# Kernel tuning notes

Measured on AMD Instinct MI355X. Metric: run time of the kernel, lower is better.

Reference implementation:

```python
import jax, jax.numpy as jnp
import numpy as np

B, D, T, G = 8, 40, 192, 256
UNITS, DEMO, OUT = 256, 16, 1


def setup_inputs() -> dict:
    key = jax.random.key(0)
    ks = jax.random.split(key, 10)
    # observation timestamps, sorted, shared across channels (per preprocessing tile)
    t1 = jnp.sort(jax.random.uniform(ks[0], (B, T)) * 48.0, axis=-1)
    times = jnp.broadcast_to(t1[:, None, :], (B, D, T))
    values = jax.random.normal(ks[1], (B, D, T))
    meas = (jax.random.uniform(ks[2], (B, D, T)) < 0.5).astype(jnp.float32)
    meas = meas.at[:, :, 0].set(1.0)  # guarantee >=1 observation per channel
    grid = jnp.broadcast_to(jnp.linspace(0.0, 48.0, G)[None, :], (B, G))
    grid_lengths = jnp.concatenate([
        jax.random.randint(ks[3], (B - 1,), G // 2, G + 1, dtype=jnp.int32),
        jnp.array([G], dtype=jnp.int32)])
    demo = jax.random.normal(ks[4], (B, DEMO))
    # learned parameters
    kernel_sic = jnp.zeros((D,))                       # softplus-param RBF widths
    cross_W = jnp.eye(D)                               # identity init
    demo_W1 = jax.random.normal(ks[5], (DEMO, UNITS)) * 0.1
    demo_b1 = jnp.zeros((UNITS,))
    demo_W2 = jax.random.normal(ks[6], (UNITS, UNITS)) * 0.05
    demo_b2 = jnp.zeros((UNITS,))
    gru_Wx = jax.random.normal(ks[7], (3 * D, 3 * UNITS)) * 0.05
    gru_Wh = jax.random.normal(ks[8], (UNITS, 3 * UNITS)) * 0.05
    gru_b = jnp.zeros((2, 3 * UNITS))                  # keras reset_after=True: [input_bias, recurrent_bias]
    out_W = jax.random.normal(ks[9], (UNITS, OUT)) * 0.1
    out_b = jnp.zeros((OUT,))
    return dict(demo=demo, times=times, values=values, measurements=meas,
                grid=grid, kernel_sic=kernel_sic, cross_W=cross_W,
                demo_W1=demo_W1, demo_b1=demo_b1, demo_W2=demo_W2, demo_b2=demo_b2,
                gru_Wx=gru_Wx, gru_Wh=gru_Wh, gru_b=gru_b,
                out_W=out_W, out_b=out_b, grid_lengths=grid_lengths)


def _forward(demo, times, values, meas, grid, kernel_sic, cross_W,
             demo_W1, demo_b1, demo_W2, demo_b2,
             gru_Wx, gru_Wh, gru_b, out_W, out_b, grid_lengths):
    # ---- single_channel_interp (reconstruction=False) ----
    logmask = jnp.where(meas > 0, 0.0, -jnp.inf)[:, :, :, None]   # [B,D,T,1]
    norm = (times[:, :, :, None] - grid[:, None, None, :]) ** 2   # [B,D,T,G]
    alpha = jax.nn.softplus(kernel_sic)[None, :, None, None]      # [1,D,1,1]

    def interp(scale):
        logits = -scale * alpha * norm + logmask                  # [B,D,T,G]
        w = jax.nn.logsumexp(logits, axis=2)                      # [B,D,G]
        p = jnp.exp(logits - w[:, :, None, :])                    # softmax over T
        y = jnp.sum(p * values[:, :, :, None], axis=2)            # [B,D,G]
        return y, w

    y, w = interp(1.0)            # smooth interpolant + log-intensity
    y_trans, _ = interp(10.0)     # sharper (transient) interpolant

    # ---- cross_channel_interp (reconstruction=False) ----
    yT = jnp.swapaxes(y, 1, 2)                                    # [B,G,D]
    wT = jnp.swapaxes(w, 1, 2)
    sw = jax.nn.softmax(wT, axis=2)                               # softmax over channels
    mean = jnp.mean(yT, axis=1, keepdims=True)                    # [B,1,D]
    rep = jnp.einsum('bgd,de->bge', sw * (yT - mean), cross_W) + mean
    rep1 = jnp.swapaxes(rep, 1, 2)                                # [B,D,G]
    intensity = jnp.exp(w)
    feats = jnp.concatenate([rep1, intensity, y_trans - rep1], axis=1)  # [B,3D,G]
    rnn_in = jnp.swapaxes(feats, 1, 2)                            # [B,G,3D]

    # ---- demo encoder -> GRU initial state ----
    h0 = jax.nn.relu(demo @ demo_W1 + demo_b1) @ demo_W2 + demo_b2

    # ---- masked GRU (keras v2, reset_after=True), return last state ----
    bi, br = gru_b[0], gru_b[1]
    Gn = rnn_in.shape[1]
    seq_mask = jnp.arange(Gn)[None, :] < grid_lengths[:, None]    # [B,G]
    x_proj = rnn_in @ gru_Wx + bi                                 # [B,G,3U]

    def step(h, inp):
        xp, m = inp                                               # [B,3U], [B]
        hp = h @ gru_Wh + br
        xz, xr, xh = jnp.split(xp, 3, axis=-1)
        hz, hr, hh = jnp.split(hp, 3, axis=-1)
        z = jax.nn.sigmoid(xz + hz)
        r = jax.nn.sigmoid(xr + hr)
        cand = jnp.tanh(xh + r * hh)
        h_new = z * h + (1.0 - z) * cand
        return jnp.where(m[:, None], h_new, h), None

    h_final, _ = jax.lax.scan(step, h0,
                              (jnp.swapaxes(x_proj, 0, 1), seq_mask.T))
    return jax.nn.sigmoid(h_final @ out_W + out_b)                # [B,OUT]


def reference(demo, times, values, measurements, grid, kernel_sic, cross_W,
              demo_W1, demo_b1, demo_W2, demo_b2,
              gru_Wx, gru_Wh, gru_b, out_W, out_b, grid_lengths):
    return _forward(demo, times, values, measurements, grid, kernel_sic, cross_W,
                    demo_W1, demo_b1, demo_W2, demo_b2,
                    gru_Wx, gru_Wh, gru_b, out_W, out_b, grid_lengths)
```

## Files before the change

### kernel.cpp

```cpp
#include <hip/hip_runtime.h>
#include <hip/hip_bf16.h>

#define B_ 8
#define D_ 40
#define T_ 192
#define G_ 256
#define U_ 768
#define H_ 256

#define PINV(x) asm volatile("" : "+v"(x))

__device__ inline float sigmoidf_(float x){
  return 1.0f/(1.0f+__expf(-x));
}
__device__ inline float tanhf_(float x){
  float ax = fabsf(x);
  float e = __expf(-2.0f*ax);
  float t = (1.0f-e)/(1.0f+e);
  return copysignf(t, x);
}
__device__ inline int sdot4(int a, int b, int c){
#if __has_builtin(__builtin_amdgcn_sdot4)
  return __builtin_amdgcn_sdot4(a, b, c, false);
#else
  int r = c;
  #pragma unroll
  for (int i=0;i<4;i++){
    int ai = (a << (24-8*i)) >> 24;
    int bi = (b << (24-8*i)) >> 24;
    r += ai*bi;
  }
  return r;
#endif
}
__device__ inline int pack4(int q0,int q1,int q2,int q3){
  return (q0&255) | ((q1&255)<<8) | ((q2&255)<<16) | ((q3&255)<<24);
}

__global__ __launch_bounds__(256) void k_interp(
    const float* __restrict__ times, const float* __restrict__ values,
    const float* __restrict__ meas, const float* __restrict__ grid,
    const float* __restrict__ ksic,
    float* __restrict__ y, float* __restrict__ w, float* __restrict__ ytr,
    float* __restrict__ mean){
  int bd = blockIdx.x;
  int b = bd / D_, d = bd % D_;
  int g = threadIdx.x;
  __shared__ float tt[T_], vv[T_], mm[T_];
  __shared__ float red[256];
  if (g < T_){
    tt[g] = times[bd*T_+g];
    vv[g] = values[bd*T_+g];
    mm[g] = meas[bd*T_+g];
  }
  __syncthreads();
  float alpha = log1pf(__expf(ksic[d]));
  float tg = grid[b*G_+g];
  float nmin = 3.4e38f;
  for (int t=0;t<T_;t++){
    if (mm[t] > 0.0f){
      float dd = tt[t]-tg;
      nmin = fminf(nmin, dd*dd);
    }
  }
  float s1=0.f, sv1=0.f, s10=0.f, sv10=0.f;
  for (int t=0;t<T_;t++){
    if (mm[t] > 0.0f){
      float dd = tt[t]-tg;
      float n = dd*dd - nmin;
      float e1  = __expf(-alpha*n);
      float e10 = __expf(-10.0f*alpha*n);
      s1 += e1;  sv1 += e1*vv[t];
      s10 += e10; sv10 += e10*vv[t];
    }
  }
  float yv = sv1/s1;
  float wv = -alpha*nmin + __logf(s1);
  y[bd*G_+g]   = yv;
  w[bd*G_+g]   = wv;
  ytr[bd*G_+g] = sv10/s10;
  red[g] = yv;
  __syncthreads();
  for (int s=128;s>0;s>>=1){
    if (g<s) red[g]+=red[g+s];
    __syncthreads();
  }
  if (g==0) mean[bd] = red[0]*(1.0f/(float)G_);
}

__global__ __launch_bounds__(256) void k_cross(
    const float* __restrict__ y, const float* __restrict__ w,
    const float* __restrict__ ytr, const float* __restrict__ mean,
    const float* __restrict__ crossW, const float* __restrict__ Wx,
    const float* __restrict__ gru_b, const int* __restrict__ lens,
    float* __restrict__ xproj){
  int blk = blockIdx.x;
  int b = blk >> 6, gq = blk & 63;
  int g0 = gq*4;
  if (g0 >= lens[b]) return;
  __shared__ float wd[4][D_], yd[4][D_], ytrd[4][D_], md[D_];
  __shared__ float cc4[4][D_], feats[4][3*D_];
  __shared__ float wstat[4][2];
  int tid = threadIdx.x;
  int gg = tid / D_;
  int d  = tid % D_;
  if (tid < 4*D_){
    int idx = (b*D_+d)*G_ + g0 + gg;
    wd[gg][d]=w[idx]; yd[gg][d]=y[idx]; ytrd[gg][d]=ytr[idx];
  }
  if (tid < D_) md[tid] = mean[b*D_+tid];
  __syncthreads();
  if (tid < 4){
    float mx=-3.4e38f;
    for (int d2=0;d2<D_;d2++) mx = fmaxf(mx, wd[tid][d2]);
    float s=0.f;
    for (int d2=0;d2<D_;d2++) s += __expf(wd[tid][d2]-mx);
    wstat[tid][0]=mx; wstat[tid][1]=1.0f/s;
  }
  __syncthreads();
  if (tid < 4*D_){
    float sw = __expf(wd[gg][d]-wstat[gg][0])*wstat[gg][1];
    cc4[gg][d] = sw*(yd[gg][d]-md[d]);
  }
  __syncthreads();
  if (tid < 4*D_){
    float acc=0.f;
    for (int d2=0;d2<D_;d2++) acc += cc4[gg][d2]*crossW[d2*D_+d];
    float rep = acc + md[d];
    feats[gg][d]       = rep;
    feats[gg][D_+d]    = __expf(wd[gg][d]);
    feats[gg][2*D_+d]  = ytrd[gg][d]-rep;
  }
  __syncthreads();
  for (int jj=0;jj<3;jj++){
    int j = tid + jj*256;
    float bi = gru_b[j];
    float a0=bi, a1=bi, a2=bi, a3=bi;
    #pragma unroll 4
    for (int i=0;i<3*D_;i++){
      float wv = Wx[i*U_+j];
      a0 += feats[0][i]*wv;
      a1 += feats[1][i]*wv;
      a2 += feats[2][i]*wv;
      a3 += feats[3][i]*wv;
    }
    size_t base = ((size_t)(b*G_+g0))*U_ + j;
    xproj[base]       = a0;
    xproj[base+U_]    = a1;
    xproj[base+2*U_]  = a2;
    xproj[base+3*U_]  = a3;
  }
}

__global__ __launch_bounds__(256) void k_demo(
    const float* __restrict__ demo, const float* __restrict__ W1,
    const float* __restrict__ b1, const float* __restrict__ W2,
    const float* __restrict__ b2, float* __restrict__ h0){
  __shared__ float dl[B_*16];
  __shared__ float hid[B_*H_];
  int u = threadIdx.x;
  if (u < B_*16) dl[u] = demo[u];
  __syncthreads();
  float acc[B_];
  #pragma unroll
  for (int b=0;b<B_;b++) acc[b]=b1[u];
  for (int i=0;i<16;i++){
    float w1 = W1[i*H_+u];
    #pragma unroll
    for (int b=0;b<B_;b++) acc[b] += dl[b*16+i]*w1;
  }
  #pragma unroll
  for (int b=0;b<B_;b++) hid[b*H_+u] = fmaxf(acc[b],0.f);
  __syncthreads();
  #pragma unroll
  for (int b=0;b<B_;b++) acc[b]=b2[u];
  for (int k=0;k<H_;k++){
    float w2 = W2[k*H_+u];
    #pragma unroll
    for (int b=0;b<B_;b++) acc[b] += hid[b*H_+k]*w2;
  }
  #pragma unroll
  for (int b=0;b<B_;b++) h0[b*H_+u]=acc[b];
}

__global__ __launch_bounds__(256) void k_quant(
    const float* __restrict__ Wh, int* __restrict__ wsq,
    float* __restrict__ wmaxs){
  int c0 = blockIdx.x*64;
  int rg = threadIdx.x >> 6;
  int cc = threadIdx.x & 63;
  int col = c0 + cc;
  float v[64];
  float mx = 0.f;
  #pragma unroll
  for (int r=0;r<64;r++){
    v[r] = Wh[(size_t)(rg*64+r)*U_ + col];
    mx = fmaxf(mx, fabsf(v[r]));
  }
  __shared__ float cm[4][64];
  cm[rg][cc] = mx;
  __syncthreads();
  float m = fmaxf(fmaxf(cm[0][cc],cm[1][cc]), fmaxf(cm[2][cc],cm[3][cc]));
  float iw = (m>0.f)? 127.0f/m : 0.f;
  if (rg==0) wmaxs[col] = m;
  #pragma unroll
  for (int k=0;k<16;k++){
    int q0=(int)rintf(v[4*k+0]*iw), q1=(int)rintf(v[4*k+1]*iw),
        q2=(int)rintf(v[4*k+2]*iw), q3=(int)rintf(v[4*k+3]*iw);
    wsq[(size_t)(rg*16+k)*U_ + col] = pack4(q0,q1,q2,q3);
  }
}

__global__ __attribute__((amdgpu_flat_work_group_size(256,256), amdgpu_waves_per_eu(1,1)))
void k_gru(
    const int* __restrict__ wsq, const float* __restrict__ wmaxs,
    const float* __restrict__ gru_b,
    const float* __restrict__ xproj, const float* __restrict__ h0,
    const int* __restrict__ lens, const float* __restrict__ outW,
    const float* __restrict__ outb, float* __restrict__ out){
  int b = blockIdx.x;
  int j = threadIdx.x;

  __shared__ __align__(16) int hq[2][64];
  __shared__ float red[H_];
  __shared__ float shs[2];

  float hj = h0[b*H_+j];
  red[j] = fabsf(hj);
  __syncthreads();
  for (int st=128; st>0; st>>=1){
    if (j < st) red[j] = fmaxf(red[j], red[j+st]);
    __syncthreads();
  }
  if (j==0){
    float bound = fmaxf(red[0], 1.0f);
    shs[0] = 127.0f/bound;
    shs[1] = bound/127.0f;
  }
  __syncthreads();
  float inv_sh = shs[0];
  float s_h    = shs[1];

  float cm0 = wmaxs[j], cm1 = wmaxs[H_+j], cm2 = wmaxs[2*H_+j];
  float fz = (cm0*(1.0f/127.0f))*s_h;
  float fr = (cm1*(1.0f/127.0f))*s_h;
  float fh = (cm2*(1.0f/127.0f))*s_h;
  float brz = gru_b[U_+j], brr = gru_b[U_+H_+j], brh = gru_b[U_+2*H_+j];

  int wqz[64], wqr[64], wqh[64];
  #pragma unroll
  for (int k=0;k<64;k++){ wqz[k] = wsq[(size_t)k*U_ + j];        PINV(wqz[k]); }
  #pragma unroll
  for (int k=0;k<64;k++){ wqr[k] = wsq[(size_t)k*U_ + H_ + j];   PINV(wqr[k]); }
  #pragma unroll
  for (int k=0;k<64;k++){ wqh[k] = wsq[(size_t)k*U_ + 2*H_ + j]; PINV(wqh[k]); }

  {
    float qf = fmaxf(-127.f, fminf(127.f, rintf(hj*inv_sh)));
    ((signed char*)hq[0])[j] = (signed char)(int)qf;
  }
  int len = lens[b];
  const float* xbase = xproj + (size_t)b*G_*U_;
  float xpz = xbase[j], xpr = xbase[H_+j], xph = xbase[2*H_+j];
  __syncthreads();

  for (int g=0; g<len; g++){
    float nxz=0.f, nxr=0.f, nxh=0.f;
    if (g+1 < len){
      const float* xn = xbase + (size_t)(g+1)*U_;
      nxz = xn[j]; nxr = xn[H_+j]; nxh = xn[2*H_+j];
    }
    const int4* hc = (const int4*)hq[g&1];
    int az=0, ar=0, ah=0;
    #pragma unroll
    for (int c=0;c<16;c++){
      int4 hv = hc[c];
      az=sdot4(hv.x,wqz[4*c+0],az); ar=sdot4(hv.x,wqr[4*c+0],ar); ah=sdot4(hv.x,wqh[4*c+0],ah);
      az=sdot4(hv.y,wqz[4*c+1],az); ar=sdot4(hv.y,wqr[4*c+1],ar); ah=sdot4(hv.y,wqh[4*c+1],ah);
      az=sdot4(hv.z,wqz[4*c+2],az); ar=sdot4(hv.z,wqr[4*c+2],ar); ah=sdot4(hv.z,wqh[4*c+2],ah);
      az=sdot4(hv.w,wqz[4*c+3],az); ar=sdot4(hv.w,wqr[4*c+3],ar); ah=sdot4(hv.w,wqh[4*c+3],ah);
    }
    float z    = sigmoidf_(xpz + brz + fz*(float)az);
    float r    = sigmoidf_(xpr + brr + fr*(float)ar);
    float cand = tanhf_(xph + r*(brh + fh*(float)ah));
    hj = z*hj + (1.0f-z)*cand;
    float qf = fmaxf(-127.f, fminf(127.f, rintf(hj*inv_sh)));
    ((signed char*)hq[(g+1)&1])[j] = (signed char)(int)qf;
    __syncthreads();
    xpz = nxz; xpr = nxr; xph = nxh;
  }

  red[j] = hj*outW[j];
  __syncthreads();
  for (int st=128;st>0;st>>=1){
    if (j<st) red[j]+=red[j+st];
    __syncthreads();
  }
  if (j==0) out[b] = sigmoidf_(red[0]+outb[0]);
}

extern "C" void kernel_launch(void* const* d_in, const int* in_sizes, int n_in,
                              void* d_out, int out_size, void* d_ws, size_t ws_size,
                              hipStream_t stream) {
  const float* demo   = (const float*)d_in[0];
  const float* times  = (const float*)d_in[1];
  const float* values = (const float*)d_in[2];
  const float* meas   = (const float*)d_in[3];
  const float* grid   = (const float*)d_in[4];
  const float* ksic   = (const float*)d_in[5];
  const float* crossW = (const float*)d_in[6];
  const float* dW1    = (const float*)d_in[7];
  const float* db1    = (const float*)d_in[8];
  const float* dW2    = (const float*)d_in[9];
  const float* db2    = (const float*)d_in[10];
  const float* gWx    = (const float*)d_in[11];
  const float* gWh    = (const float*)d_in[12];
  const float* gb     = (const float*)d_in[13];
  const float* outW   = (const float*)d_in[14];
  const float* outb   = (const float*)d_in[15];
  const int*   lens   = (const int*)d_in[16];
  float* out = (float*)d_out;

  float* ws   = (float*)d_ws;
  float* y    = ws;
  float* w    = y    + B_*D_*G_;
  float* ytr  = w    + B_*D_*G_;
  float* mean = ytr  + B_*D_*G_;
  float* h0   = mean + B_*D_;
  float* xprj = h0   + B_*H_;
  int*   wsq  = (int*)(xprj + (size_t)B_*G_*U_);
  float* wmx  = (float*)(wsq + 64*U_);

  k_interp<<<B_*D_, 256, 0, stream>>>(times, values, meas, grid, ksic, y, w, ytr, mean);
  k_quant <<<12,    256, 0, stream>>>(gWh, wsq, wmx);
  k_demo  <<<1,     256, 0, stream>>>(demo, dW1, db1, dW2, db2, h0);
  k_cross <<<B_*64, 256, 0, stream>>>(y, w, ytr, mean, crossW, gWx, gb, lens, xprj);
  k_gru   <<<B_,    256, 0, stream>>>(wsq, wmx, gb, xprj, h0, lens, outW, outb, out);
}
```

Measured before the change: 283.6 us.

## Batch GRU recurrence into one block using int8 MFMA over all sequences

The GRU recurrence now runs all 8 batch sequences in a single workgroup. The per-step hidden-by-weight product is done with int8 MFMA 16x16x64 instructions, replacing per-thread sdot4 loops. Weights are prepacked into MFMA fragment layout, and the input projection is stored as fp16 in a step-major interleaved layout that is double-buffered through LDS. Recurrent biases for z and r are folded into the projection. Risks: it always runs all 256 steps with masking instead of stopping at each sequence's length, fp16 loses precision on the projection, and k_cross skips writing steps past each length, so those xls entries stay uninitialised.

```diff
diff --git a/kernel.cpp b/kernel.cpp
--- a/kernel.cpp
+++ b/kernel.cpp
@@ -7,8 +7,11 @@
 #define G_ 256
 #define U_ 768
 #define H_ 256
-
-#define PINV(x) asm volatile("" : "+v"(x))
+#define XSTEP 6144
+
+typedef int v4i __attribute__((ext_vector_type(4)));
+typedef float f32x4 __attribute__((ext_vector_type(4)));
+typedef _Float16 f16x4 __attribute__((ext_vector_type(4)));
 
 __device__ inline float sigmoidf_(float x){
   return 1.0f/(1.0f+__expf(-x));
@@ -19,22 +22,18 @@
   float t = (1.0f-e)/(1.0f+e);
   return copysignf(t, x);
 }
-__device__ inline int sdot4(int a, int b, int c){
-#if __has_builtin(__builtin_amdgcn_sdot4)
-  return __builtin_amdgcn_sdot4(a, b, c, false);
-#else
-  int r = c;
-  #pragma unroll
-  for (int i=0;i<4;i++){
-    int ai = (a << (24-8*i)) >> 24;
-    int bi = (b << (24-8*i)) >> 24;
-    r += ai*bi;
-  }
-  return r;
-#endif
-}
 __device__ inline int pack4(int q0,int q1,int q2,int q3){
   return (q0&255) | ((q1&255)<<8) | ((q2&255)<<16) | ((q3&255)<<24);
+}
+__device__ inline v4i mfma_i8(v4i a, v4i b, v4i c){
+#if __has_builtin(__builtin_amdgcn_mfma_i32_16x16x64_i8)
+  return __builtin_amdgcn_mfma_i32_16x16x64_i8(a, b, c, 0, 0, 0);
+#else
+  v4i d;
+  asm volatile("v_mfma_i32_16x16x64_i8 %0, %1, %2, %3\n\ts_nop 7\n\ts_nop 7"
+               : "=v"(d) : "v"(a), "v"(b), "v"(c));
+  return d;
+#endif
 }
 
 __global__ __launch_bounds__(256) void k_interp(
@@ -93,7 +92,7 @@
     const float* __restrict__ ytr, const float* __restrict__ mean,
     const float* __restrict__ crossW, const float* __restrict__ Wx,
     const float* __restrict__ gru_b, const int* __restrict__ lens,
-    float* __restrict__ xproj){
+    _Float16* __restrict__ xls){
   int blk = blockIdx.x;
   int b = blk >> 6, gq = blk & 63;
   int g0 = gq*4;
@@ -132,23 +131,24 @@
     feats[gg][2*D_+d]  = ytrd[gg][d]-rep;
   }
   __syncthreads();
+  int n = tid >> 4, jl2 = tid & 15;
   for (int jj=0;jj<3;jj++){
-    int j = tid + jj*256;
-    float bi = gru_b[j];
+    int colg = jj*256 + tid;
+    float bi = gru_b[colg] + ((jj<2)? gru_b[U_+colg] : 0.0f);
     float a0=bi, a1=bi, a2=bi, a3=bi;
     #pragma unroll 4
     for (int i=0;i<3*D_;i++){
-      float wv = Wx[i*U_+j];
+      float wv = Wx[i*U_+colg];
       a0 += feats[0][i]*wv;
       a1 += feats[1][i]*wv;
       a2 += feats[2][i]*wv;
       a3 += feats[3][i]*wv;
     }
-    size_t base = ((size_t)(b*G_+g0))*U_ + j;
-    xproj[base]       = a0;
-    xproj[base+U_]    = a1;
-    xproj[base+2*U_]  = a2;
-    xproj[base+3*U_]  = a3;
+    size_t off = (size_t)(n*16 + jl2)*24 + jj*8 + b;
+    xls[(size_t)(g0+0)*XSTEP + off] = (_Float16)a0;
+    xls[(size_t)(g0+1)*XSTEP + off] = (_Float16)a1;
+    xls[(size_t)(g0+2)*XSTEP + off] = (_Float16)a2;
+    xls[(size_t)(g0+3)*XSTEP + off] = (_Float16)a3;
   }
 }
 
@@ -184,119 +184,223 @@
 }
 
 __global__ __launch_bounds__(256) void k_quant(
-    const float* __restrict__ Wh, int* __restrict__ wsq,
+    const float* __restrict__ Wh, int* __restrict__ wfrag,
     float* __restrict__ wmaxs){
-  int c0 = blockIdx.x*64;
-  int rg = threadIdx.x >> 6;
-  int cc = threadIdx.x & 63;
-  int col = c0 + cc;
-  float v[64];
-  float mx = 0.f;
-  #pragma unroll
-  for (int r=0;r<64;r++){
-    v[r] = Wh[(size_t)(rg*64+r)*U_ + col];
-    mx = fmaxf(mx, fabsf(v[r]));
-  }
+  int bid = blockIdx.x;
+  int c0 = bid*64;
+  int gate = c0 >> 8;
+  int n0 = (c0 & 255) >> 4;
   __shared__ float cm[4][64];
-  cm[rg][cc] = mx;
-  __syncthreads();
-  float m = fmaxf(fmaxf(cm[0][cc],cm[1][cc]), fmaxf(cm[2][cc],cm[3][cc]));
-  float iw = (m>0.f)? 127.0f/m : 0.f;
-  if (rg==0) wmaxs[col] = m;
-  #pragma unroll
-  for (int k=0;k<16;k++){
-    int q0=(int)rintf(v[4*k+0]*iw), q1=(int)rintf(v[4*k+1]*iw),
-        q2=(int)rintf(v[4*k+2]*iw), q3=(int)rintf(v[4*k+3]*iw);
-    wsq[(size_t)(rg*16+k)*U_ + col] = pack4(q0,q1,q2,q3);
+  __shared__ float mcomb[64];
+  {
+    int rg = threadIdx.x >> 6, cc = threadIdx.x & 63;
+    int col = c0 + cc;
+    float mx = 0.f;
+    for (int r = 0; r < 64; r++)
+      mx = fmaxf(mx, fabsf(Wh[(size_t)(rg*64+r)*U_ + col]));
+    cm[rg][cc] = mx;
+  }
+  __syncthreads();
+  if (threadIdx.x < 64){
+    int cc = threadIdx.x;
+    float m = fmaxf(fmaxf(cm[0][cc],cm[1][cc]), fmaxf(cm[2][cc],cm[3][cc]));
+    mcomb[cc] = m;
+    wmaxs[c0+cc] = m;
+  }
+  __syncthreads();
+  int nn = threadIdx.x >> 6;
+  int L  = threadIdx.x & 63;
+  int jl = L & 15, qq = L >> 4;
+  int col = c0 + 16*nn + jl;
+  float m = mcomb[16*nn + jl];
+  float iw = (m > 0.f) ? 127.0f/m : 0.f;
+  int n = n0 + nn;
+  #pragma unroll
+  for (int kk = 0; kk < 4; kk++){
+    #pragma unroll
+    for (int dw = 0; dw < 4; dw++){
+      int k0 = 64*kk + qq*16 + 4*dw;
+      int qa = (int)rintf(Wh[(size_t)(k0+0)*U_+col]*iw);
+      int qb = (int)rintf(Wh[(size_t)(k0+1)*U_+col]*iw);
+      int qc = (int)rintf(Wh[(size_t)(k0+2)*U_+col]*iw);
+      int qd = (int)rintf(Wh[(size_t)(k0+3)*U_+col]*iw);
+      wfrag[(((n*3+gate)*4+kk)*64 + L)*4 + dw] = pack4(qa,qb,qc,qd);
+    }
   }
 }
 
 __global__ __attribute__((amdgpu_flat_work_group_size(256,256), amdgpu_waves_per_eu(1,1)))
 void k_gru(
-    const int* __restrict__ wsq, const float* __restrict__ wmaxs,
-    const float* __restrict__ gru_b,
-    const float* __restrict__ xproj, const float* __restrict__ h0,
-    const int* __restrict__ lens, const float* __restrict__ outW,
-    const float* __restrict__ outb, float* __restrict__ out){
-  int b = blockIdx.x;
-  int j = threadIdx.x;
-
-  __shared__ __align__(16) int hq[2][64];
-  __shared__ float red[H_];
-  __shared__ float shs[2];
-
-  float hj = h0[b*H_+j];
-  red[j] = fabsf(hj);
-  __syncthreads();
-  for (int st=128; st>0; st>>=1){
-    if (j < st) red[j] = fmaxf(red[j], red[j+st]);
+    const int* __restrict__ wfrag, const float* __restrict__ wmaxs,
+    const float* __restrict__ gru_b, const _Float16* __restrict__ xls,
+    const float* __restrict__ h0, const int* __restrict__ lens,
+    const float* __restrict__ outW, const float* __restrict__ outb,
+    float* __restrict__ out){
+  int tid = threadIdx.x;
+  int w = tid >> 6, L = tid & 63;
+  int jl = L & 15, q2 = L >> 4;
+  int qh = q2 & 1;
+
+  __shared__ _Float16 xbuf[2][XSTEP];
+  __shared__ signed char hqs[2][16][272];
+  __shared__ __align__(16) float hf[256][8];
+  __shared__ float shsA[8][2];
+  __shared__ float redq[8][64];
+
+  for (int i = tid; i < (int)(2*16*272/4); i += 256) ((int*)hqs)[i] = 0;
+
+  if (tid < 8){
+    float m = 0.f;
+    for (int j = 0; j < H_; j++) m = fmaxf(m, fabsf(h0[tid*H_ + j]));
+    float bound = fmaxf(m, 1.0f);
+    shsA[tid][0] = 127.0f/bound;
+    shsA[tid][1] = bound/127.0f;
+  }
+  __syncthreads();
+
+  {
+    int j = tid;
+    #pragma unroll
+    for (int b = 0; b < 8; b++){
+      float h = h0[b*H_ + j];
+      hf[j][b] = h;
+      float qf = fmaxf(-127.f, fminf(127.f, rintf(h*shsA[b][0])));
+      hqs[0][b][j] = (signed char)(int)qf;
+    }
+  }
+
+  v4i wreg[4][3][4];
+  #pragma unroll
+  for (int t = 0; t < 4; t++){
+    int n = w*4 + t;
+    #pragma unroll
+    for (int gg = 0; gg < 3; gg++){
+      #pragma unroll
+      for (int kk = 0; kk < 4; kk++){
+        wreg[t][gg][kk] = *(const v4i*)(wfrag + (((n*3+gg)*4+kk)*64 + L)*4);
+      }
+    }
+  }
+  float fz[4], fr2[4], fh2[4], brh[4];
+  #pragma unroll
+  for (int t = 0; t < 4; t++){
+    int j = 16*(w*4+t) + jl;
+    fz[t]  = wmaxs[j]      * (1.0f/127.0f);
+    fr2[t] = wmaxs[H_+j]   * (1.0f/127.0f);
+    fh2[t] = wmaxs[2*H_+j] * (1.0f/127.0f);
+    brh[t] = gru_b[U_ + 2*H_ + j];
+  }
+  float shv[4], ishv[4]; int lenv[4];
+  #pragma unroll
+  for (int rr = 0; rr < 4; rr++){
+    int b = qh*4 + rr;
+    shv[rr]  = shsA[b][1];
+    ishv[rr] = shsA[b][0];
+    lenv[rr] = lens[b];
+  }
+
+  {
+    const _Float16* src = xls + (size_t)w*1536 + L*8;
+    f16x4 r0=*(const f16x4*)(src),      r1=*(const f16x4*)(src+4);
+    f16x4 r2=*(const f16x4*)(src+512),  r3=*(const f16x4*)(src+516);
+    f16x4 r4=*(const f16x4*)(src+1024), r5=*(const f16x4*)(src+1028);
+    _Float16* dst = &xbuf[0][w*1536 + L*8];
+    *(f16x4*)(dst)=r0;      *(f16x4*)(dst+4)=r1;
+    *(f16x4*)(dst+512)=r2;  *(f16x4*)(dst+516)=r3;
+    *(f16x4*)(dst+1024)=r4; *(f16x4*)(dst+1028)=r5;
+  }
+  __syncthreads();
+
+  int cur = 0;
+  for (int g = 0; g < G_; g++){
+    int nxt = cur ^ 1;
+    f16x4 xr0,xr1,xr2,xr3,xr4,xr5;
+    {
+      int gn = (g+1 < G_) ? g+1 : g;
+      const _Float16* src = xls + (size_t)gn*XSTEP + w*1536 + L*8;
+      xr0=*(const f16x4*)(src);      xr1=*(const f16x4*)(src+4);
+      xr2=*(const f16x4*)(src+512);  xr3=*(const f16x4*)(src+516);
+      xr4=*(const f16x4*)(src+1024); xr5=*(const f16x4*)(src+1028);
+    }
+    v4i a0 = *(const v4i*)(&hqs[cur][jl][q2*16]);
+    v4i a1 = *(const v4i*)(&hqs[cur][jl][64 + q2*16]);
+    v4i a2 = *(const v4i*)(&hqs[cur][jl][128 + q2*16]);
+    v4i a3 = *(const v4i*)(&hqs[cur][jl][192 + q2*16]);
+
+    #pragma unroll
+    for (int t = 0; t < 4; t++){
+      v4i accz = {0,0,0,0}, accr = {0,0,0,0}, acch = {0,0,0,0};
+      accz = mfma_i8(a0, wreg[t][0][0], accz);
+      accz = mfma_i8(a1, wreg[t][0][1], accz);
+      accz = mfma_i8(a2, wreg[t][0][2], accz);
+      accz = mfma_i8(a3, wreg[t][0][3], accz);
+      accr = mfma_i8(a0, wreg[t][1][0], accr);
+      accr = mfma_i8(a1, wreg[t][1][1], accr);
+      accr = mfma_i8(a2, wreg[t][1][2], accr);
+      accr = mfma_i8(a3, wreg[t][1][3], accr);
+      acch = mfma_i8(a0, wreg[t][2][0], acch);
+      acch = mfma_i8(a1, wreg[t][2][1], acch);
+      acch = mfma_i8(a2, wreg[t][2][2], acch);
+      acch = mfma_i8(a3, wreg[t][2][3], acch);
+
+      const _Float16* xb = &xbuf[cur][(size_t)w*1536 + (t*16 + jl)*24];
+      f16x4 xz4 = *(const f16x4*)(xb + 0*8 + qh*4);
+      f16x4 xr4g= *(const f16x4*)(xb + 1*8 + qh*4);
+      f16x4 xh4 = *(const f16x4*)(xb + 2*8 + qh*4);
+      int j = 16*(w*4+t) + jl;
+      f32x4 hold = *(const f32x4*)(&hf[j][qh*4]);
+      float hn[4];
+      #pragma unroll
+      for (int rr = 0; rr < 4; rr++){
+        float dz = fz[t]  * shv[rr] * (float)accz[rr];
+        float dr = fr2[t] * shv[rr] * (float)accr[rr];
+        float dh = fh2[t] * shv[rr] * (float)acch[rr];
+        float z    = sigmoidf_((float)xz4[rr] + dz);
+        float r    = sigmoidf_((float)xr4g[rr] + dr);
+        float cand = tanhf_((float)xh4[rr] + r*(brh[t] + dh));
+        float hv = hold[rr];
+        float h2 = z*hv + (1.0f-z)*cand;
+        hn[rr] = (g < lenv[rr]) ? h2 : hv;
+      }
+      if (q2 < 2){
+        f32x4 hw = {hn[0],hn[1],hn[2],hn[3]};
+        *(f32x4*)(&hf[j][qh*4]) = hw;
+        #pragma unroll
+        for (int rr = 0; rr < 4; rr++){
+          float qf = fmaxf(-127.f, fminf(127.f, rintf(hn[rr]*ishv[rr])));
+          hqs[nxt][qh*4+rr][j] = (signed char)(int)qf;
+        }
+      }
+    }
+    {
+      _Float16* dst = &xbuf[nxt][w*1536 + L*8];
+      *(f16x4*)(dst)=xr0;      *(f16x4*)(dst+4)=xr1;
+      *(f16x4*)(dst+512)=xr2;  *(f16x4*)(dst+516)=xr3;
+      *(f16x4*)(dst+1024)=xr4; *(f16x4*)(dst+1028)=xr5;
+    }
     __syncthreads();
-  }
-  if (j==0){
-    float bound = fmaxf(red[0], 1.0f);
-    shs[0] = 127.0f/bound;
-    shs[1] = bound/127.0f;
-  }
-  __syncthreads();
-  float inv_sh = shs[0];
-  float s_h    = shs[1];
-
-  float cm0 = wmaxs[j], cm1 = wmaxs[H_+j], cm2 = wmaxs[2*H_+j];
-  float fz = (cm0*(1.0f/127.0f))*s_h;
-  float fr = (cm1*(1.0f/127.0f))*s_h;
-  float fh = (cm2*(1.0f/127.0f))*s_h;
-  float brz = gru_b[U_+j], brr = gru_b[U_+H_+j], brh = gru_b[U_+2*H_+j];
-
-  int wqz[64], wqr[64], wqh[64];
-  #pragma unroll
-  for (int k=0;k<64;k++){ wqz[k] = wsq[(size_t)k*U_ + j];        PINV(wqz[k]); }
-  #pragma unroll
-  for (int k=0;k<64;k++){ wqr[k] = wsq[(size_t)k*U_ + H_ + j];   PINV(wqr[k]); }
-  #pragma unroll
-  for (int k=0;k<64;k++){ wqh[k] = wsq[(size_t)k*U_ + 2*H_ + j]; PINV(wqh[k]); }
-
-  {
-    float qf = fmaxf(-127.f, fminf(127.f, rintf(hj*inv_sh)));
-    ((signed char*)hq[0])[j] = (signed char)(int)qf;
-  }
-  int len = lens[b];
-  const float* xbase = xproj + (size_t)b*G_*U_;
-  float xpz = xbase[j], xpr = xbase[H_+j], xph = xbase[2*H_+j];
-  __syncthreads();
-
-  for (int g=0; g<len; g++){
-    float nxz=0.f, nxr=0.f, nxh=0.f;
-    if (g+1 < len){
-      const float* xn = xbase + (size_t)(g+1)*U_;
-      nxz = xn[j]; nxr = xn[H_+j]; nxh = xn[2*H_+j];
-    }
-    const int4* hc = (const int4*)hq[g&1];
-    int az=0, ar=0, ah=0;
-    #pragma unroll
-    for (int c=0;c<16;c++){
-      int4 hv = hc[c];
-      az=sdot4(hv.x,wqz[4*c+0],az); ar=sdot4(hv.x,wqr[4*c+0],ar); ah=sdot4(hv.x,wqh[4*c+0],ah);
-      az=sdot4(hv.y,wqz[4*c+1],az); ar=sdot4(hv.y,wqr[4*c+1],ar); ah=sdot4(hv.y,wqh[4*c+1],ah);
-      az=sdot4(hv.z,wqz[4*c+2],az); ar=sdot4(hv.z,wqr[4*c+2],ar); ah=sdot4(hv.z,wqh[4*c+2],ah);
-      az=sdot4(hv.w,wqz[4*c+3],az); ar=sdot4(hv.w,wqr[4*c+3],ar); ah=sdot4(hv.w,wqh[4*c+3],ah);
-    }
-    float z    = sigmoidf_(xpz + brz + fz*(float)az);
-    float r    = sigmoidf_(xpr + brr + fr*(float)ar);
-    float cand = tanhf_(xph + r*(brh + fh*(float)ah));
-    hj = z*hj + (1.0f-z)*cand;
-    float qf = fmaxf(-127.f, fminf(127.f, rintf(hj*inv_sh)));
-    ((signed char*)hq[(g+1)&1])[j] = (signed char)(int)qf;
-    __syncthreads();
-    xpz = nxz; xpr = nxr; xph = nxh;
-  }
-
-  red[j] = hj*outW[j];
-  __syncthreads();
-  for (int st=128;st>0;st>>=1){
-    if (j<st) red[j]+=red[j+st];
-    __syncthreads();
-  }
-  if (j==0) out[b] = sigmoidf_(red[0]+outb[0]);
+    cur = nxt;
+  }
+
+  float part[4] = {0.f,0.f,0.f,0.f};
+  #pragma unroll
+  for (int t = 0; t < 4; t++){
+    int j = 16*(w*4+t) + jl;
+    float ow = outW[j];
+    f32x4 hv = *(const f32x4*)(&hf[j][qh*4]);
+    part[0] += hv[0]*ow; part[1] += hv[1]*ow;
+    part[2] += hv[2]*ow; part[3] += hv[3]*ow;
+  }
+  if (q2 < 2){
+    #pragma unroll
+    for (int rr = 0; rr < 4; rr++) redq[qh*4+rr][w*16 + jl] = part[rr];
+  }
+  __syncthreads();
+  if (tid < 8){
+    float s = 0.f;
+    for (int i = 0; i < 64; i++) s += redq[tid][i];
+    out[tid] = sigmoidf_(s + outb[0]);
+  }
 }
 
 extern "C" void kernel_launch(void* const* d_in, const int* in_sizes, int n_in,
@@ -327,13 +431,13 @@
   float* ytr  = w    + B_*D_*G_;
   float* mean = ytr  + B_*D_*G_;
   float* h0   = mean + B_*D_;
-  float* xprj = h0   + B_*H_;
-  int*   wsq  = (int*)(xprj + (size_t)B_*G_*U_);
-  float* wmx  = (float*)(wsq + 64*U_);
+  _Float16* xls = (_Float16*)(h0 + B_*H_);
+  int*   wfrag = (int*)(xls + (size_t)G_*XSTEP);
+  float* wmx   = (float*)(wfrag + 16*3*4*64*4);
 
   k_interp<<<B_*D_, 256, 0, stream>>>(times, values, meas, grid, ksic, y, w, ytr, mean);
-  k_quant <<<12,    256, 0, stream>>>(gWh, wsq, wmx);
+  k_quant <<<12,    256, 0, stream>>>(gWh, wfrag, wmx);
   k_demo  <<<1,     256, 0, stream>>>(demo, dW1, db1, dW2, db2, h0);
-  k_cross <<<B_*64, 256, 0, stream>>>(y, w, ytr, mean, crossW, gWx, gb, lens, xprj);
-  k_gru   <<<B_,    256, 0, stream>>>(wsq, wmx, gb, xprj, h0, lens, outW, outb, out);
-}
+  k_cross <<<B_*64, 256, 0, stream>>>(y, w, ytr, mean, crossW, gWx, gb, lens, xls);
+  k_gru   <<<1,     256, 0, stream>>>(wfrag, wmx, gb, xls, h0, lens, outW, outb, out);
+}
```

After: 851.7 us. 3x slower.

## Split GRU gates across three thread groups per batch block

Applied to the files above, without the earlier changes.

The recurrent GRU kernel now launches 768 threads per batch block instead of 256. Each thread holds the int8 weights for one gate column (64 regs instead of 192) and computes one dot product. The r and h gate results are exchanged through shared memory, and the first 256 threads apply the gate update. This shortens the serial dot-product chain per step and cuts register pressure. The cost is a second __syncthreads per timestep and extra shared-memory traffic.

```diff
diff --git a/kernel.cpp b/kernel.cpp
--- a/kernel.cpp
+++ b/kernel.cpp
@@ -7,8 +7,6 @@
 #define G_ 256
 #define U_ 768
 #define H_ 256
-
-#define PINV(x) asm volatile("" : "+v"(x))
 
 __device__ inline float sigmoidf_(float x){
   return 1.0f/(1.0f+__expf(-x));
@@ -211,7 +209,7 @@
   }
 }
 
-__global__ __attribute__((amdgpu_flat_work_group_size(256,256), amdgpu_waves_per_eu(1,1)))
+__global__ __attribute__((amdgpu_flat_work_group_size(768,768), amdgpu_waves_per_eu(3,3)))
 void k_gru(
     const int* __restrict__ wsq, const float* __restrict__ wmaxs,
     const float* __restrict__ gru_b,
@@ -219,20 +217,28 @@
     const int* __restrict__ lens, const float* __restrict__ outW,
     const float* __restrict__ outb, float* __restrict__ out){
   int b = blockIdx.x;
-  int j = threadIdx.x;
+  int t = threadIdx.x;
+  int gt = t >> 8;
+  int j  = t & 255;
 
   __shared__ __align__(16) int hq[2][64];
+  __shared__ float sPre[H_];
+  __shared__ float hPre[H_];
+  __shared__ float xhv[H_];
   __shared__ float red[H_];
   __shared__ float shs[2];
 
-  float hj = h0[b*H_+j];
-  red[j] = fabsf(hj);
+  float hj = 0.f;
+  if (t < H_){
+    hj = h0[b*H_+t];
+    red[t] = fabsf(hj);
+  }
   __syncthreads();
   for (int st=128; st>0; st>>=1){
-    if (j < st) red[j] = fmaxf(red[j], red[j+st]);
-    __syncthreads();
-  }
-  if (j==0){
+    if (t < st) red[t] = fmaxf(red[t], red[t+st]);
+    __syncthreads();
+  }
+  if (t==0){
     float bound = fmaxf(red[0], 1.0f);
     shs[0] = 127.0f/bound;
     shs[1] = bound/127.0f;
@@ -241,62 +247,58 @@
   float inv_sh = shs[0];
   float s_h    = shs[1];
 
-  float cm0 = wmaxs[j], cm1 = wmaxs[H_+j], cm2 = wmaxs[2*H_+j];
-  float fz = (cm0*(1.0f/127.0f))*s_h;
-  float fr = (cm1*(1.0f/127.0f))*s_h;
-  float fh = (cm2*(1.0f/127.0f))*s_h;
-  float brz = gru_b[U_+j], brr = gru_b[U_+H_+j], brh = gru_b[U_+2*H_+j];
-
-  int wqz[64], wqr[64], wqh[64];
-  #pragma unroll
-  for (int k=0;k<64;k++){ wqz[k] = wsq[(size_t)k*U_ + j];        PINV(wqz[k]); }
-  #pragma unroll
-  for (int k=0;k<64;k++){ wqr[k] = wsq[(size_t)k*U_ + H_ + j];   PINV(wqr[k]); }
-  #pragma unroll
-  for (int k=0;k<64;k++){ wqh[k] = wsq[(size_t)k*U_ + 2*H_ + j]; PINV(wqh[k]); }
-
-  {
+  float fc = wmaxs[t]*(1.0f/127.0f)*s_h;
+  float br = gru_b[U_ + t];
+
+  int wq[64];
+  #pragma unroll
+  for (int k=0;k<64;k++) wq[k] = wsq[(size_t)k*U_ + t];
+
+  if (t < H_){
     float qf = fmaxf(-127.f, fminf(127.f, rintf(hj*inv_sh)));
-    ((signed char*)hq[0])[j] = (signed char)(int)qf;
+    ((signed char*)hq[0])[t] = (signed char)(int)qf;
   }
   int len = lens[b];
   const float* xbase = xproj + (size_t)b*G_*U_;
-  float xpz = xbase[j], xpr = xbase[H_+j], xph = xbase[2*H_+j];
+  float xp = xbase[t];
   __syncthreads();
 
   for (int g=0; g<len; g++){
-    float nxz=0.f, nxr=0.f, nxh=0.f;
-    if (g+1 < len){
-      const float* xn = xbase + (size_t)(g+1)*U_;
-      nxz = xn[j]; nxr = xn[H_+j]; nxh = xn[2*H_+j];
-    }
+    float nx = 0.f;
+    if (g+1 < len) nx = xbase[(size_t)(g+1)*U_ + t];
     const int4* hc = (const int4*)hq[g&1];
-    int az=0, ar=0, ah=0;
+    int a0=0, a1=0, a2=0;
     #pragma unroll
-    for (int c=0;c<16;c++){
-      int4 hv = hc[c];
-      az=sdot4(hv.x,wqz[4*c+0],az); ar=sdot4(hv.x,wqr[4*c+0],ar); ah=sdot4(hv.x,wqh[4*c+0],ah);
-      az=sdot4(hv.y,wqz[4*c+1],az); ar=sdot4(hv.y,wqr[4*c+1],ar); ah=sdot4(hv.y,wqh[4*c+1],ah);
-      az=sdot4(hv.z,wqz[4*c+2],az); ar=sdot4(hv.z,wqr[4*c+2],ar); ah=sdot4(hv.z,wqh[4*c+2],ah);
-      az=sdot4(hv.w,wqz[4*c+3],az); ar=sdot4(hv.w,wqr[4*c+3],ar); ah=sdot4(hv.w,wqh[4*c+3],ah);
-    }
-    float z    = sigmoidf_(xpz + brz + fz*(float)az);
-    float r    = sigmoidf_(xpr + brr + fr*(float)ar);
-    float cand = tanhf_(xph + r*(brh + fh*(float)ah));
-    hj = z*hj + (1.0f-z)*cand;
-    float qf = fmaxf(-127.f, fminf(127.f, rintf(hj*inv_sh)));
-    ((signed char*)hq[(g+1)&1])[j] = (signed char)(int)qf;
-    __syncthreads();
-    xpz = nxz; xpr = nxr; xph = nxh;
-  }
-
-  red[j] = hj*outW[j];
+    for (int c=0;c<8;c++){
+      int4 u = hc[2*c], v = hc[2*c+1];
+      a0=sdot4(u.x,wq[8*c+0],a0); a1=sdot4(u.y,wq[8*c+1],a1); a2=sdot4(u.z,wq[8*c+2],a2);
+      a0=sdot4(u.w,wq[8*c+3],a0); a1=sdot4(v.x,wq[8*c+4],a1); a2=sdot4(v.y,wq[8*c+5],a2);
+      a0=sdot4(v.z,wq[8*c+6],a0); a1=sdot4(v.w,wq[8*c+7],a1);
+    }
+    float dot = fc*(float)((a0+a1)+a2);
+    if (gt == 1)      sPre[j] = xp + br + dot;
+    else if (gt == 2){ hPre[j] = br + dot; xhv[j] = xp; }
+    float myz = xp + br + dot;
+    __syncthreads();
+    if (gt == 0){
+      float z    = sigmoidf_(myz);
+      float r    = sigmoidf_(sPre[j]);
+      float cand = tanhf_(xhv[j] + r*hPre[j]);
+      hj = z*hj + (1.0f-z)*cand;
+      float qf = fmaxf(-127.f, fminf(127.f, rintf(hj*inv_sh)));
+      ((signed char*)hq[(g+1)&1])[j] = (signed char)(int)qf;
+    }
+    __syncthreads();
+    xp = nx;
+  }
+
+  if (t < H_) red[t] = hj*outW[t];
   __syncthreads();
   for (int st=128;st>0;st>>=1){
-    if (j<st) red[j]+=red[j+st];
-    __syncthreads();
-  }
-  if (j==0) out[b] = sigmoidf_(red[0]+outb[0]);
+    if (t<st) red[t]+=red[t+st];
+    __syncthreads();
+  }
+  if (t==0) out[b] = sigmoidf_(red[0]+outb[0]);
 }
 
 extern "C" void kernel_launch(void* const* d_in, const int* in_sizes, int n_in,
@@ -335,5 +337,5 @@
   k_quant <<<12,    256, 0, stream>>>(gWh, wsq, wmx);
   k_demo  <<<1,     256, 0, stream>>>(demo, dW1, db1, dW2, db2, h0);
   k_cross <<<B_*64, 256, 0, stream>>>(y, w, ytr, mean, crossW, gWx, gb, lens, xprj);
-  k_gru   <<<B_,    256, 0, stream>>>(wsq, wmx, gb, xprj, h0, lens, outW, outb, out);
-}
+  k_gru   <<<B_,    768, 0, stream>>>(wsq, wmx, gb, xprj, h0, lens, outW, outb, out);
+}
```

Measured after the change: 285.2 us. No clear change (+0.5%).
